# Performance work log

Measured on AMD Instinct MI355X. Metric: run time of the kernel, lower is better.

The kernel has to match this reference:

```python
import jax, jax.numpy as jnp
import numpy as np

B, T, NI, NH, NO = 256, 512, 512, 2048, 256

def setup_inputs() -> dict:
    key = jax.random.key(0)
    ks = jax.random.split(key, 7)
    def lin(kw, kb, fan_in, shape_w, shape_b):
        bound = 1.0 / np.sqrt(fan_in)
        W = jax.random.uniform(kw, shape_w, jnp.float32, -bound, bound)
        b = jax.random.uniform(kb, shape_b, jnp.float32, -bound, bound)
        return W, b
    x = jax.random.normal(ks[0], (B, T, NI), jnp.float32)
    W_enc, b_enc = lin(ks[1], ks[2], NI, (NH, NI), (NH,))
    W_rec, b_rec = lin(ks[3], ks[4], NH, (NH, NH), (NH,))
    W_dec, b_dec = lin(ks[5], ks[6], NH, (NO, NH), (NO,))
    dt = jnp.array([0.5], jnp.float32)
    a = jnp.array([1.0], jnp.float32)
    return {"x": x, "dt": dt, "a": a,
            "W_enc": W_enc, "b_enc": b_enc,
            "W_rec": W_rec, "b_rec": b_rec,
            "W_dec": W_dec, "b_dec": b_dec}

def reference(x, dt, a, W_enc, b_enc, W_rec, b_rec, W_dec, b_dec):
    # x: [B, T, NI] -> time-major [T, B, NI]
    s = jax.nn.sigmoid(dt)                      # (1,) gate, broadcasts
    xt = jnp.swapaxes(x, 0, 1)                  # [T, B, NI]
    # Encoder applied to all timesteps at once (same math as per-step Linear)
    enc = jnp.einsum('tbi,hi->tbh', xt, W_enc) + b_enc  # [T, B, NH]
    h0 = jnp.zeros((x.shape[0], W_rec.shape[0]), x.dtype)  # [B, NH]
    def step(h, e_t):
        h = (1.0 - s) * h + s * a * jnp.tanh(e_t + h @ W_rec.T + b_rec)
        y_t = h @ W_dec.T + b_dec               # [B, NO]
        return h, y_t
    h_final, y = jax.lax.scan(step, h0, enc)    # y: [T, B, NO]
    return y, h_final[None]                     # h: [1, B, NH] as in torch
```

## Files before the change

kernel.cpp:

```cpp
#include <hip/hip_runtime.h>
#include <hip/hip_bf16.h>
#include <math.h>


#define B_   256
#define T_   512
#define NI_  512
#define NH_  2048
#define NO_  256

typedef __bf16 bf16_t;
typedef __bf16 bf16x8 __attribute__((ext_vector_type(8)));
typedef float  f32x4  __attribute__((ext_vector_type(4)));

#define MFMA16(a,b,c) __builtin_amdgcn_mfma_f32_16x16x32_bf16((a),(b),(c),0,0,0)
#define XCC_HWREG_IMM (20 | (31 << 11))

__device__ __forceinline__ void ld_sc0_x4(bf16x8& d, const void* p) {
  asm volatile("global_load_dwordx4 %0, %1, off sc0" : "=v"(d) : "v"(p));
}
__device__ __forceinline__ void ld_sc01_u32(unsigned& d, const void* p) {
  asm volatile("global_load_dword %0, %1, off sc0 sc1" : "=v"(d) : "v"(p));
}
__device__ __forceinline__ void st_sc01_u32(void* p, unsigned v) {
  asm volatile("global_store_dword %0, %1, off sc0 sc1" :: "v"(p), "v"(v));
}
#define WAIT_VM0() do { asm volatile("s_waitcnt vmcnt(0)" ::: "memory"); \
                        __builtin_amdgcn_sched_barrier(0); } while (0)
#define WAIT_VM(n) do { asm volatile("s_waitcnt vmcnt(" #n ")" ::: "memory"); \
                        __builtin_amdgcn_sched_barrier(0); } while (0)

__device__ __forceinline__ void spin_ge(int* p, int tgt) {
  while (__hip_atomic_load(p, __ATOMIC_RELAXED, __HIP_MEMORY_SCOPE_AGENT) < tgt)
    __builtin_amdgcn_s_sleep(4);
}
__device__ __forceinline__ void bump(int* p) {
  __hip_atomic_fetch_add(p, 1, __ATOMIC_RELAXED, __HIP_MEMORY_SCOPE_AGENT);
}

__device__ __forceinline__ int* s_floc(int* s, int x)  { return s + x*16; }
__device__ __forceinline__ int* s_fmir(int* s, int x)  { return s + 128 + x*16; }
__device__ __forceinline__ int* s_fpub(int* s, int i)  { return s + 256 + i*16; }
__device__ __forceinline__ int* s_reg(int* s, int x)   { return s + 384 + x*16; }
__device__ __forceinline__ int* s_start(int* s)        { return s + 512; }

__global__ __launch_bounds__(256) void k_cvt(const float* __restrict__ src,
                                             bf16_t* __restrict__ dst, int n) {
  int i = blockIdx.x * 256 + threadIdx.x;
  const int stride = gridDim.x * 256;
  for (; i < n; i += stride) dst[i] = (bf16_t)src[i];
}

__device__ __forceinline__ void dec_tile(
    int tid, int side, int rank, int rg,
    const bf16_t* hl, const bf16_t* hm,
    const bf16_t* __restrict__ Wdec, const float* __restrict__ b_dec,
    float* __restrict__ y_out, float* Scr)
{
  const int lane = tid & 63, w = tid >> 6, fl = lane & 15, kg = lane >> 4;
  const int drl = side*32 + (rank >> 4)*16;
  const int dc  = (rank & 15) * 16;
  const bf16_t* hbase = ((w >> 3) == side) ? hl : hm;
  const int kb = (w & 7) * 128;
  bf16x8 hf[4];
  #pragma unroll
  for (int i = 0; i < 4; ++i)
    ld_sc0_x4(hf[i], hbase + (size_t)(drl + fl)*1024 + kb + i*32 + kg*8);
  WAIT_VM0();
  f32x4 d = {0.f, 0.f, 0.f, 0.f};
  #pragma unroll
  for (int i = 0; i < 4; ++i) {
    bf16x8 wf = *reinterpret_cast<const bf16x8*>(
        Wdec + (size_t)(dc + fl)*NH_ + w*128 + i*32 + kg*8);
    d = MFMA16(hf[i], wf, d);
  }
  __syncthreads();
  #pragma unroll
  for (int j = 0; j < 4; ++j) Scr[w*256 + (kg*4 + j)*16 + fl] = d[j];
  __syncthreads();
  if (tid < 256) {
    const int r = tid >> 4, c = tid & 15;
    float s = b_dec[dc + c];
    #pragma unroll
    for (int ww = 0; ww < 16; ++ww) s += Scr[ww*256 + r*16 + c];
    y_out[(size_t)(rg*64 + drl + r)*NO_ + dc + c] = s;
  }
}

__global__ __launch_bounds__(1024, 1) void k_prnn(
    const float* __restrict__ x,
    const float* __restrict__ dt_p, const float* __restrict__ a_p,
    const float* __restrict__ Wrec,
    const bf16_t* __restrict__ Wenc_b, const bf16_t* __restrict__ Wdec_b,
    const float* __restrict__ b_rec, const float* __restrict__ b_enc,
    const float* __restrict__ b_dec,
    bf16_t* __restrict__ hloc, bf16_t* __restrict__ hmir,
    bf16_t* __restrict__ pub, int* __restrict__ sync_,
    float* __restrict__ out)
{
  __shared__ alignas(16) bf16x8 Wl[256 * 32];
  __shared__ alignas(16) float  Scr[6144];
  __shared__ alignas(16) bf16_t Ts[2048];
  __shared__ int sh_xcd, sh_rank;

  const int tid  = threadIdx.x;
  const int lane = tid & 63;
  const int fl   = lane & 15;
  const int kg   = lane >> 4;
  const int w    = tid >> 6;
  const int rt   = w & 3;
  const int kq   = w >> 2;

  if (tid == 0) {
    const int xc = (int)(__builtin_amdgcn_s_getreg(XCC_HWREG_IMM) & 7u);
    const int rk = __hip_atomic_fetch_add(s_reg(sync_, xc), 1,
                     __ATOMIC_RELAXED, __HIP_MEMORY_SCOPE_AGENT);
    bump(s_start(sync_));
    spin_ge(s_start(sync_), 256);
    sh_xcd = xc; sh_rank = rk;
  }
  __syncthreads();
  const int xcd = sh_xcd, rank = sh_rank;
  if (rank >= 32) return;
  const int rg = xcd >> 1, side = xcd & 1;

  bf16_t* hloc_x = hloc + (size_t)xcd * 4 * 65536;
  bf16_t* hmir_x = hmir + (size_t)xcd * 4 * 65536;
  bf16_t* pub_own = pub + (size_t)(rg*2 + side)   * 2 * 65536;
  bf16_t* pub_par = pub + (size_t)(rg*2 + (side^1)) * 2 * 65536;
  int* floc = s_floc(sync_, xcd);
  int* fmir = s_fmir(sync_, xcd);
  int* fpub_o = s_fpub(sync_, rg*2 + side);
  int* fpub_p = s_fpub(sync_, rg*2 + (side^1));

  const float sgate = 1.f / (1.f + expf(-dt_p[0]));
  const float av = a_p[0];
  const float gi = 1.f - sgate;
  const float sav = sgate * av;
  const int colbase = rank * 32;
  const int colg0 = side*1024 + colbase + fl;
  const int colg1 = colg0 + 16;
  const float bias0 = b_rec[colg0] + b_enc[colg0];
  const float bias1 = b_rec[colg1] + b_enc[colg1];
  const bf16_t* we0 = Wenc_b + (size_t)colg0 * NI_;
  const bf16_t* we1 = Wenc_b + (size_t)colg1 * NI_;
  const int lrow = rt*16 + fl;
  const int grow = rg*64 + lrow;

  f32x4 hr0 = {0.f,0.f,0.f,0.f}, hr1 = {0.f,0.f,0.f,0.f};

  {
    const int c = tid >> 5, part = tid & 31;
    const int cglob = side*1024 + colbase + c;
    #pragma unroll
    for (int i = 0; i < 8; ++i) {
      const int g = part*8 + i;
      const float* src = Wrec + (size_t)cglob * NH_ + g*8;
      float4 f0 = reinterpret_cast<const float4*>(src)[0];
      float4 f1 = reinterpret_cast<const float4*>(src)[1];
      bf16x8 w8 = {(bf16_t)f0.x, (bf16_t)f0.y, (bf16_t)f0.z, (bf16_t)f0.w,
                   (bf16_t)f1.x, (bf16_t)f1.y, (bf16_t)f1.z, (bf16_t)f1.w};
      Wl[g*32 + c] = w8;
    }
  }
  __syncthreads();

  #pragma unroll 1
  for (int t = 0; t < T_; ++t) {
    const int slotR = (t + 3) & 3;
    const int slotW = t & 3;
    const int pslot = t & 1;

    if (tid == 0)  spin_ge(floc, 32*t);
    if (tid == 64) spin_ge(fmir, 32*t);
    __syncthreads();

    const bf16_t* hl = hloc_x + (size_t)slotR * 65536;
    const bf16_t* hm = hmir_x + (size_t)slotR * 65536;

    f32x4 acc0 = {0.f,0.f,0.f,0.f}, acc1 = {0.f,0.f,0.f,0.f};
    const int kbase = kq * 640;
    if (kq < 3) {
      bf16x8 pa[4];
      auto aptr = [&](int c) -> const bf16_t* {
        const int k = kbase + c*32;
        const bf16_t* b = ((k >> 10) == side) ? hl : hm;
        return b + (size_t)lrow*1024 + (k & 1023) + kg*8;
      };
      ld_sc0_x4(pa[0], aptr(0)); ld_sc0_x4(pa[1], aptr(1));
      ld_sc0_x4(pa[2], aptr(2)); ld_sc0_x4(pa[3], aptr(3));
      #pragma unroll 4
      for (int c = 0; c < 16; ++c) {
        WAIT_VM(3);
        const int gg = kbase/8 + c*4 + kg;
        acc0 = MFMA16(pa[c & 3], Wl[gg*32 + fl], acc0);
        acc1 = MFMA16(pa[c & 3], Wl[gg*32 + 16 + fl], acc1);
        ld_sc0_x4(pa[c & 3], aptr(c + 4));
      }
      #pragma unroll
      for (int c = 16; c < 20; ++c) {
        switch (19 - c) { case 3: WAIT_VM(3); break; case 2: WAIT_VM(2); break;
                          case 1: WAIT_VM(1); break; default: WAIT_VM0(); }
        const int gg = kbase/8 + c*4 + kg;
        acc0 = MFMA16(pa[c & 3], Wl[gg*32 + fl], acc0);
        acc1 = MFMA16(pa[c & 3], Wl[gg*32 + 16 + fl], acc1);
      }
    } else {
      const bf16_t* bh = (1 == side) ? hl : hm;
      bf16x8 pa[4];
      #pragma unroll
      for (int c = 0; c < 4; ++c)
        ld_sc0_x4(pa[c], bh + (size_t)lrow*1024 + ((1920 + c*32) & 1023) + kg*8);
      #pragma unroll
      for (int c = 0; c < 4; ++c) {
        switch (3 - c) { case 3: WAIT_VM(3); break; case 2: WAIT_VM(2); break;
                         case 1: WAIT_VM(1); break; default: WAIT_VM0(); }
        const int gg = 240 + c*4 + kg;
        acc0 = MFMA16(pa[c], Wl[gg*32 + fl], acc0);
        acc1 = MFMA16(pa[c], Wl[gg*32 + 16 + fl], acc1);
      }
      const float* xrow = x + ((size_t)grow * T_ + t) * NI_;
      #pragma unroll 4
      for (int c = 0; c < 16; ++c) {
        const int kp = c*32 + kg*8;
        float4 u = *reinterpret_cast<const float4*>(xrow + kp);
        float4 v = *reinterpret_cast<const float4*>(xrow + kp + 4);
        bf16x8 a = {(bf16_t)u.x, (bf16_t)u.y, (bf16_t)u.z, (bf16_t)u.w,
                    (bf16_t)v.x, (bf16_t)v.y, (bf16_t)v.z, (bf16_t)v.w};
        bf16x8 b0 = *reinterpret_cast<const bf16x8*>(we0 + kp);
        bf16x8 b1 = *reinterpret_cast<const bf16x8*>(we1 + kp);
        acc0 = MFMA16(a, b0, acc0);
        acc1 = MFMA16(a, b1, acc1);
      }
    }

    __syncthreads();
    if (kq != 0) {
      const int base = (kq - 1)*2048 + rt*16*32;
      #pragma unroll
      for (int j = 0; j < 4; ++j) {
        Scr[base + (kg*4 + j)*32 + fl]      = acc0[j];
        Scr[base + (kg*4 + j)*32 + 16 + fl] = acc1[j];
      }
    }
    __syncthreads();
    if (kq == 0) {
      #pragma unroll
      for (int j = 0; j < 4; ++j) {
        const int ri = (rt*16 + kg*4 + j)*32;
        const float v0 = acc0[j] + Scr[ri + fl] + Scr[2048 + ri + fl] + Scr[4096 + ri + fl];
        const float v1 = acc1[j] + Scr[ri + 16 + fl] + Scr[2048 + ri + 16 + fl] + Scr[4096 + ri + 16 + fl];
        const float o0 = gi*hr0[j] + sav*tanhf(v0 + bias0);
        const float o1 = gi*hr1[j] + sav*tanhf(v1 + bias1);
        hr0[j] = o0; hr1[j] = o1;
        Ts[(rt*16 + kg*4 + j)*32 + fl]      = (bf16_t)o0;
        Ts[(rt*16 + kg*4 + j)*32 + 16 + fl] = (bf16_t)o1;
        if (t == T_ - 1) {
          float* hd = out + (size_t)T_*B_*NO_ + (size_t)(rg*64 + rt*16 + kg*4 + j)*NH_;
          hd[colg0] = o0; hd[colg1] = o1;
        }
      }
    }
    __syncthreads();

    {
      const int r = tid >> 4, q = tid & 15;
      const unsigned dv = *reinterpret_cast<const unsigned*>(&Ts[r*32 + q*2]);
      const int off = r*1024 + colbase + q*2;
      *reinterpret_cast<unsigned*>(hloc_x + (size_t)slotW*65536 + off) = dv;
      st_sc01_u32(pub_own + (size_t)pslot*65536 + off, dv);
      WAIT_VM0();
    }
    __syncthreads();
    if (tid == 0) { bump(floc); bump(fpub_o); }

    if (tid == 0) spin_ge(fpub_p, 32*(t + 1));
    __syncthreads();
    {
      const int r = tid >> 4, q = tid & 15;
      const int off = r*1024 + colbase + q*2;
      unsigned mv;
      ld_sc01_u32(mv, pub_par + (size_t)pslot*65536 + off);
      WAIT_VM0();
      *reinterpret_cast<unsigned*>(hmir_x + (size_t)slotW*65536 + off) = mv;
    }
    __syncthreads();
    if (tid == 0) bump(fmir);

    if (t >= 2)
      dec_tile(tid, side, rank, rg,
               hloc_x + (size_t)((t + 2) & 3)*65536,
               hmir_x + (size_t)((t + 2) & 3)*65536,
               Wdec_b, b_dec, out + (size_t)(t - 2)*B_*NO_, Scr);
  }

  if (tid == 0)  spin_ge(floc, 32*T_);
  if (tid == 64) spin_ge(fmir, 32*T_);
  __syncthreads();
  dec_tile(tid, side, rank, rg, hloc_x + (size_t)2*65536, hmir_x + (size_t)2*65536,
           Wdec_b, b_dec, out + (size_t)(T_ - 2)*B_*NO_, Scr);
  dec_tile(tid, side, rank, rg, hloc_x + (size_t)3*65536, hmir_x + (size_t)3*65536,
           Wdec_b, b_dec, out + (size_t)(T_ - 1)*B_*NO_, Scr);
}

extern "C" void kernel_launch(void* const* d_in, const int* in_sizes, int n_in,
                              void* d_out, int out_size, void* d_ws, size_t ws_size,
                              hipStream_t stream) {
  const float* x     = (const float*)d_in[0];
  const float* dt_p  = (const float*)d_in[1];
  const float* a_p   = (const float*)d_in[2];
  const float* W_enc = (const float*)d_in[3];
  const float* b_enc = (const float*)d_in[4];
  const float* W_rec = (const float*)d_in[5];
  const float* b_rec = (const float*)d_in[6];
  const float* W_dec = (const float*)d_in[7];
  const float* b_dec = (const float*)d_in[8];
  float* out = (float*)d_out;

  char* p = (char*)d_ws;
  bf16_t* hloc   = (bf16_t*)p;  p += (size_t)8*4*65536*2;
  bf16_t* hmir   = (bf16_t*)p;  p += (size_t)8*4*65536*2;
  bf16_t* pub    = (bf16_t*)p;  p += (size_t)8*2*65536*2;
  bf16_t* Wenc_b = (bf16_t*)p;  p += (size_t)NH_*NI_*2;
  bf16_t* Wdec_b = (bf16_t*)p;  p += (size_t)NO_*NH_*2;
  int*    sync_  = (int*)p;     p += 8192;

  hipMemsetAsync(hloc, 0, (size_t)8*4*65536*2, stream);
  hipMemsetAsync(hmir, 0, (size_t)8*4*65536*2, stream);
  hipMemsetAsync(sync_, 0, 8192, stream);

  k_cvt<<<128, 256, 0, stream>>>(W_enc, Wenc_b, NH_ * NI_);
  k_cvt<<<64, 256, 0, stream>>>(W_dec, Wdec_b, NO_ * NH_);

  k_prnn<<<dim3(256), dim3(1024), 0, stream>>>(
      x, dt_p, a_p, W_rec, Wenc_b, Wdec_b, b_rec, b_enc, b_dec,
      hloc, hmir, pub, sync_, out);
}
```

Measured before the change: 13.43 ms.

## Use per-block flags instead of shared counters and overlap decoder with partner wait

Each block now gets its own cache-line-separated flag instead of all blocks doing atomic adds on one shared counter per XCD. Waiters spread the polling across 32 lanes, one per producer flag. The decoder tile for step t-2 now runs between publishing the hidden state and waiting for the partner XCD's data, hiding part of the cross-XCD wait. The spin sleep is also shortened. The costs are more polling traffic and a larger sync area.

After: 12.99 ms. 3.3% less time.

```diff
diff --git a/kernel.cpp b/kernel.cpp
--- a/kernel.cpp
+++ b/kernel.cpp
@@ -32,17 +32,15 @@
 
 __device__ __forceinline__ void spin_ge(int* p, int tgt) {
   while (__hip_atomic_load(p, __ATOMIC_RELAXED, __HIP_MEMORY_SCOPE_AGENT) < tgt)
-    __builtin_amdgcn_s_sleep(4);
+    __builtin_amdgcn_s_sleep(2);
 }
 __device__ __forceinline__ void bump(int* p) {
   __hip_atomic_fetch_add(p, 1, __ATOMIC_RELAXED, __HIP_MEMORY_SCOPE_AGENT);
 }
 
-__device__ __forceinline__ int* s_floc(int* s, int x)  { return s + x*16; }
-__device__ __forceinline__ int* s_fmir(int* s, int x)  { return s + 128 + x*16; }
-__device__ __forceinline__ int* s_fpub(int* s, int i)  { return s + 256 + i*16; }
-__device__ __forceinline__ int* s_reg(int* s, int x)   { return s + 384 + x*16; }
-__device__ __forceinline__ int* s_start(int* s)        { return s + 512; }
+__device__ __forceinline__ int* fA_loc(int* s, int x, int r) { return s + (x*32 + r)*16; }
+__device__ __forceinline__ int* fA_mir(int* s, int x, int r) { return s + 4096 + (x*32 + r)*16; }
+__device__ __forceinline__ int* fA_pub(int* s, int x, int r) { return s + 8192 + (x*32 + r)*16; }
 
 __global__ __launch_bounds__(256) void k_cvt(const float* __restrict__ src,
                                              bf16_t* __restrict__ dst, int n) {
@@ -113,10 +111,10 @@
 
   if (tid == 0) {
     const int xc = (int)(__builtin_amdgcn_s_getreg(XCC_HWREG_IMM) & 7u);
-    const int rk = __hip_atomic_fetch_add(s_reg(sync_, xc), 1,
-                     __ATOMIC_RELAXED, __HIP_MEMORY_SCOPE_AGENT);
-    bump(s_start(sync_));
-    spin_ge(s_start(sync_), 256);
+    int* reg = sync_ + 12288 + xc * 16;
+    const int rk = __hip_atomic_fetch_add(reg, 1, __ATOMIC_RELAXED, __HIP_MEMORY_SCOPE_AGENT);
+    __hip_atomic_fetch_add(sync_ + 12416, 1, __ATOMIC_RELAXED, __HIP_MEMORY_SCOPE_AGENT);
+    spin_ge(sync_ + 12416, 256);
     sh_xcd = xc; sh_rank = rk;
   }
   __syncthreads();
@@ -126,12 +124,8 @@
 
   bf16_t* hloc_x = hloc + (size_t)xcd * 4 * 65536;
   bf16_t* hmir_x = hmir + (size_t)xcd * 4 * 65536;
-  bf16_t* pub_own = pub + (size_t)(rg*2 + side)   * 2 * 65536;
-  bf16_t* pub_par = pub + (size_t)(rg*2 + (side^1)) * 2 * 65536;
-  int* floc = s_floc(sync_, xcd);
-  int* fmir = s_fmir(sync_, xcd);
-  int* fpub_o = s_fpub(sync_, rg*2 + side);
-  int* fpub_p = s_fpub(sync_, rg*2 + (side^1));
+  bf16_t* pub_own = pub + (size_t)xcd * 2 * 65536;
+  bf16_t* pub_par = pub + (size_t)(xcd ^ 1) * 2 * 65536;
 
   const float sgate = 1.f / (1.f + expf(-dt_p[0]));
   const float av = a_p[0];
@@ -171,8 +165,8 @@
     const int slotW = t & 3;
     const int pslot = t & 1;
 
-    if (tid == 0)  spin_ge(floc, 32*t);
-    if (tid == 64) spin_ge(fmir, 32*t);
+    if (tid < 32)                    spin_ge(fA_loc(sync_, xcd, tid), t);
+    else if (tid >= 64 && tid < 96)  spin_ge(fA_mir(sync_, xcd, tid - 64), t);
     __syncthreads();
 
     const bf16_t* hl = hloc_x + (size_t)slotR * 65536;
@@ -249,7 +243,8 @@
       for (int j = 0; j < 4; ++j) {
         const int ri = (rt*16 + kg*4 + j)*32;
         const float v0 = acc0[j] + Scr[ri + fl] + Scr[2048 + ri + fl] + Scr[4096 + ri + fl];
-        const float v1 = acc1[j] + Scr[ri + 16 + fl] + Scr[2048 + ri + 16 + fl] + Scr[4096 + ri + 16 + fl];
+        const float v1 = acc1[j] + Scr[ri + 16 + fl] + Scr[2048 + ri + 16 + fl]
+                                 + Scr[4096 + ri + 16 + fl];
         const float o0 = gi*hr0[j] + sav*tanhf(v0 + bias0);
         const float o1 = gi*hr1[j] + sav*tanhf(v1 + bias1);
         hr0[j] = o0; hr1[j] = o1;
@@ -272,9 +267,16 @@
       WAIT_VM0();
     }
     __syncthreads();
-    if (tid == 0) { bump(floc); bump(fpub_o); }
-
-    if (tid == 0) spin_ge(fpub_p, 32*(t + 1));
+    if (tid == 0)       bump(fA_loc(sync_, xcd, rank));
+    else if (tid == 64) bump(fA_pub(sync_, xcd, rank));
+
+    if (t >= 2)
+      dec_tile(tid, side, rank, rg,
+               hloc_x + (size_t)((t + 2) & 3)*65536,
+               hmir_x + (size_t)((t + 2) & 3)*65536,
+               Wdec_b, b_dec, out + (size_t)(t - 2)*B_*NO_, Scr);
+
+    if (tid == 0) spin_ge(fA_pub(sync_, xcd ^ 1, rank), t + 1);
     __syncthreads();
     {
       const int r = tid >> 4, q = tid & 15;
@@ -285,17 +287,11 @@
       *reinterpret_cast<unsigned*>(hmir_x + (size_t)slotW*65536 + off) = mv;
     }
     __syncthreads();
-    if (tid == 0) bump(fmir);
-
-    if (t >= 2)
-      dec_tile(tid, side, rank, rg,
-               hloc_x + (size_t)((t + 2) & 3)*65536,
-               hmir_x + (size_t)((t + 2) & 3)*65536,
-               Wdec_b, b_dec, out + (size_t)(t - 2)*B_*NO_, Scr);
-  }
-
-  if (tid == 0)  spin_ge(floc, 32*T_);
-  if (tid == 64) spin_ge(fmir, 32*T_);
+    if (tid == 0) bump(fA_mir(sync_, xcd, rank));
+  }
+
+  if (tid < 32)                    spin_ge(fA_loc(sync_, xcd, tid), T_);
+  else if (tid >= 64 && tid < 96)  spin_ge(fA_mir(sync_, xcd, tid - 64), T_);
   __syncthreads();
   dec_tile(tid, side, rank, rg, hloc_x + (size_t)2*65536, hmir_x + (size_t)2*65536,
            Wdec_b, b_dec, out + (size_t)(T_ - 2)*B_*NO_, Scr);
@@ -323,11 +319,11 @@
   bf16_t* pub    = (bf16_t*)p;  p += (size_t)8*2*65536*2;
   bf16_t* Wenc_b = (bf16_t*)p;  p += (size_t)NH_*NI_*2;
   bf16_t* Wdec_b = (bf16_t*)p;  p += (size_t)NO_*NH_*2;
-  int*    sync_  = (int*)p;     p += 8192;
+  int*    sync_  = (int*)p;     p += 16384*4;
 
   hipMemsetAsync(hloc, 0, (size_t)8*4*65536*2, stream);
   hipMemsetAsync(hmir, 0, (size_t)8*4*65536*2, stream);
-  hipMemsetAsync(sync_, 0, 8192, stream);
+  hipMemsetAsync(sync_, 0, 16384*4, stream);
 
   k_cvt<<<128, 256, 0, stream>>>(W_enc, Wenc_b, NH_ * NI_);
   k_cvt<<<64, 256, 0, stream>>>(W_dec, Wdec_b, NO_ * NH_);
```
